# Optimization experiments

Measured on AMD Instinct MI355X. Metric: run time of the kernel, lower is better.

Reference implementation:

```python
import jax, jax.numpy as jnp
import numpy as np
from jax import lax

DILS = [2 ** i for i in range(11)] * 3  # 33 layers


def _conv1(x, w, b):
    # kernel_size=1 conv: w (O,I), x (B,I,T)
    return jnp.einsum('oi,bit->bot', w, x) + b[None, :, None]


def _dconv2(x, w, b, d):
    # kernel_size=2 dilated conv, torch padding='same': pad (d//2, d-d//2)
    y = lax.conv_general_dilated(
        x, w, window_strides=(1,), padding=[(d // 2, d - d // 2)],
        rhs_dilation=(d,), dimension_numbers=('NCH', 'OIH', 'NCH'))
    return y + b[None, :, None]


def setup_inputs() -> dict:
    key = jax.random.key(0)
    ks = jax.random.split(key, 7)
    B, T = 32, 16384
    s1 = 1.0           # fan_in=1*1
    s16 = 1.0 / np.sqrt(16.0)
    s16k2 = 1.0 / np.sqrt(16.0 * 2)
    s32 = 1.0 / np.sqrt(32.0)
    return {
        'x': jax.random.normal(ks[0], (B, 1, T), jnp.float32),
        'w1_first': jax.random.normal(ks[1], (16, 1), jnp.float32) * s1,
        'b1_first': jnp.zeros((16,), jnp.float32),
        'w1_post': jax.random.normal(ks[2], (32, 16, 16), jnp.float32) * s16,
        'b1_post': jnp.zeros((32, 16), jnp.float32),
        'wf': jax.random.normal(ks[3], (33, 32, 16, 2), jnp.float32) * s16k2,
        'bf': jnp.zeros((33, 32), jnp.float32),
        'wg': jax.random.normal(ks[4], (33, 32, 16, 2), jnp.float32) * s16k2,
        'bg': jnp.zeros((33, 32), jnp.float32),
        'w2': jax.random.normal(ks[5], (33, 16, 32), jnp.float32) * s32,
        'b2': jnp.zeros((33, 16), jnp.float32),
    }


def reference(x, w1_first, b1_first, w1_post, b1_post, wf, bf, wg, bg, w2, b2):
    skip_sum = 0.0
    for i, d in enumerate(DILS):
        if i == 0:
            x = jax.nn.relu(_conv1(x, w1_first, b1_first))
        else:
            x = jax.nn.relu(_conv1(x, w1_post[i - 1], b1_post[i - 1]))
        x_f = _dconv2(x, wf[i], bf[i], d)
        x_g = _dconv2(x, wg[i], bg[i], d)
        z = jnp.tanh(x_f) * jax.nn.sigmoid(x_g)
        z = jax.nn.relu(_conv1(z, w2[i], b2[i]))
        x = x + z
        skip_sum = skip_sum + z
    return jax.nn.relu(skip_sum)
```

## Files before the change

kernel.cpp:

```cpp
#include <hip/hip_runtime.h>

#define BB 32
#define TT 16384

typedef __attribute__((ext_vector_type(8))) short bf16x8;
typedef __attribute__((ext_vector_type(4))) float f32x4;
typedef __attribute__((ext_vector_type(4))) int i32x4;

#define MFMA(A, B, C) __builtin_amdgcn_mfma_f32_16x16x32_bf16((A), (B), (C), 0, 0, 0)

__device__ __forceinline__ unsigned short bf16_rne(float f) {
    unsigned int u = __float_as_uint(f);
    return (unsigned short)((u + 0x7FFF + ((u >> 16) & 1)) >> 16);
}
__device__ __forceinline__ float bf16_to_f(unsigned short h) {
    return __uint_as_float(((unsigned int)h) << 16);
}
__device__ __forceinline__ uint2 pk4(f32x4 v) {
    uint2 r;
    asm("v_cvt_pk_bf16_f32 %0, %1, %2" : "=v"(r.x) : "v"(v[0]), "v"(v[1]));
    asm("v_cvt_pk_bf16_f32 %0, %1, %2" : "=v"(r.y) : "v"(v[2]), "v"(v[3]));
    return r;
}

__device__ __forceinline__ float fast_sigmoid(float x) {
    float e = __expf(-x);
    return __builtin_amdgcn_rcpf(1.0f + e);
}
__device__ __forceinline__ float fast_tanh(float x) {
    float ax = fabsf(x);
    float e = __expf(2.0f * ax);
    float r = 1.0f - 2.0f * __builtin_amdgcn_rcpf(1.0f + e);
    return copysignf(r, x);
}

__global__ void prep_kernel(const float* __restrict__ w1_first,
                            const float* __restrict__ b1_first,
                            const float* __restrict__ w1_post,
                            const float* __restrict__ b1_post,
                            const float* __restrict__ wf, const float* __restrict__ bfb,
                            const float* __restrict__ wg, const float* __restrict__ bgb,
                            const float* __restrict__ w2, const float* __restrict__ b2,
                            short* __restrict__ Wfrag, float* __restrict__ Bset) {
    int L = blockIdx.x;
    int l = threadIdx.x;
    int op = l & 15;
    int q = l >> 4;
    int i0 = (q & 1) << 3;
    int tap = q >> 1;

    float gbuf[6][8];
#pragma unroll
    for (int j = 0; j < 8; ++j) {
        gbuf[0][j] = (L == 0) ? 0.f
                   : w1_post[((size_t)(L - 1) * 16 + op) * 16 + i0 + j];
        gbuf[1][j] = wf[(((size_t)L * 32 + op) * 16 + i0 + j) * 2 + tap];
        gbuf[2][j] = wf[(((size_t)L * 32 + 16 + op) * 16 + i0 + j) * 2 + tap];
        gbuf[3][j] = wg[(((size_t)L * 32 + op) * 16 + i0 + j) * 2 + tap];
        gbuf[4][j] = wg[(((size_t)L * 32 + 16 + op) * 16 + i0 + j) * 2 + tap];
        gbuf[5][j] = w2[((size_t)L * 16 + op) * 32 + (q << 3) + j];
    }

    constexpr int gsel[7] = {0, 0, 1, 2, 3, 4, 5};
    constexpr int hsel[7] = {1, 0, 1, 1, 1, 1, 1};
#pragma unroll
    for (int f = 0; f < 7; ++f) {
        size_t base = (((size_t)L * 7 + f) * 64 + l) * 8;
#pragma unroll
        for (int j = 0; j < 8; ++j) {
            float v = gbuf[gsel[f]][j];
            unsigned short h = bf16_rne(v);
            Wfrag[base + j] = hsel[f] ? (short)h
                                      : (short)bf16_rne(v - bf16_to_f(h));
        }
    }

#pragma unroll
    for (int r = 0; r < 4; ++r) {
        int c = (q << 2) + r;
        float bv[6];
        bv[0] = (L == 0) ? b1_first[c] : b1_post[(size_t)(L - 1) * 16 + c];
        bv[1] = bfb[(size_t)L * 32 + c];
        bv[2] = bfb[(size_t)L * 32 + 16 + c];
        bv[3] = bgb[(size_t)L * 32 + c];
        bv[4] = bgb[(size_t)L * 32 + 16 + c];
        bv[5] = b2[(size_t)L * 16 + c];
#pragma unroll
        for (int s = 0; s < 6; ++s)
            Bset[(((size_t)L * 6 + s) * 64 + l) * 4 + r] = bv[s];
    }
}

__device__ __forceinline__ f32x4 conv1_eval(bool first, const void* __restrict__ xin,
                                            const float* __restrict__ w1f,
                                            int b, int tp, int q,
                                            f32x4 b1v, bf16x8 A12) {
    const f32x4 zero = {0.f, 0.f, 0.f, 0.f};
    bool valid = ((unsigned)tp) < (unsigned)TT;
    f32x4 acc = valid ? b1v : zero;
    if (first) {
        const float* xf = (const float*)xin;
        float xv = valid ? xf[(size_t)b * TT + tp] : 0.f;
        const float4* w4 = (const float4*)w1f;
        float4 w = w4[q];
        acc[0] = fmaf(w.x, xv, acc[0]);
        acc[1] = fmaf(w.y, xv, acc[1]);
        acc[2] = fmaf(w.z, xv, acc[2]);
        acc[3] = fmaf(w.w, xv, acc[3]);
    } else {
        int tpc = valid ? tp : 0;
        const bf16x8 z8 = {0, 0, 0, 0, 0, 0, 0, 0};
        const bf16x8* xp = (const bf16x8*)((const char*)xin +
                            ((size_t)b * TT + tpc) * 32 + ((q & 1) << 4));
        bf16x8 bb = valid ? *xp : z8;
        acc = MFMA(A12, bb, acc);
    }
#pragma unroll
    for (int r = 0; r < 4; ++r) acc[r] = fmaxf(acc[r], 0.f);
    return acc;
}

template <int MODE>
__global__ __launch_bounds__(256) void wn_layer(
    const void* __restrict__ xin, void* __restrict__ xout,
    float* __restrict__ skip, float* __restrict__ dout,
    const short* __restrict__ WfragL, const float* __restrict__ BsetL,
    const float* __restrict__ w1f, int d) {
    __shared__ char sm[8192];

    const int tid = threadIdx.x;
    const int wave = tid >> 6, lane = tid & 63;
    const int p = lane & 15, q = lane >> 4;

    const int blk = ((blockIdx.x & 7) << 10) + (blockIdx.x >> 3);
    const int b = blk >> 8;
    const int tbase = ((blk & 255) << 6) + (wave << 4);
    const int pl = d >> 1, pr = d - pl;

    char* xrb = sm + wave * 1024;
    char* zb = sm + 4096 + wave * 1024;
    const int xorb = (p & 8) << 2;

    const bf16x8* WF = (const bf16x8*)WfragL;
    const f32x4* BS = (const f32x4*)BsetL;

    const f32x4 b1v = BS[lane];
    bf16x8 A12 = {0, 0, 0, 0, 0, 0, 0, 0};
    if (MODE != 1) A12 = (q < 2) ? WF[lane] : WF[64 + lane];

#pragma unroll
    for (int g = 0; g < 2; ++g) {
        int ts = tbase + (g ? pr : -pl);
        f32x4 xr = conv1_eval(MODE == 1, xin, w1f, b, ts + p, q, b1v, A12);
        *(uint2*)(xrb + (g << 9) +
                  ((((q >> 1) << 8) + (p << 4) + ((q & 1) << 3)) ^ xorb)) = pk4(xr);
    }

    f32x4 xrC = {0.f, 0.f, 0.f, 0.f};
    if (MODE != 2)
        xrC = conv1_eval(MODE == 1, xin, w1f, b, tbase + p, q, b1v, A12);

    bf16x8 bxr = *(const bf16x8*)(xrb + ((q >> 1) << 9) +
                                  ((((q & 1) << 8) + (p << 4)) ^ xorb));
    f32x4 f0 = MFMA(WF[2 * 64 + lane], bxr, BS[64 + lane]);
    f32x4 f1 = MFMA(WF[3 * 64 + lane], bxr, BS[128 + lane]);
    f32x4 g0 = MFMA(WF[4 * 64 + lane], bxr, BS[192 + lane]);
    f32x4 g1 = MFMA(WF[5 * 64 + lane], bxr, BS[256 + lane]);

    f32x4 z0, z1;
#pragma unroll
    for (int r = 0; r < 4; ++r) {
        z0[r] = fast_tanh(f0[r]) * fast_sigmoid(g0[r]);
        z1[r] = fast_tanh(f1[r]) * fast_sigmoid(g1[r]);
    }
    {
        int base = (((q >> 1) << 8) + (p << 4) + ((q & 1) << 3)) ^ xorb;
        *(uint2*)(zb + base) = pk4(z0);
        *(uint2*)(zb + 512 + base) = pk4(z1);
    }

    bf16x8 bz = *(const bf16x8*)(zb + (((q << 8) + (p << 4)) ^ xorb));
    f32x4 z2 = MFMA(WF[6 * 64 + lane], bz, BS[320 + lane]);
#pragma unroll
    for (int r = 0; r < 4; ++r) z2[r] = fmaxf(z2[r], 0.f);

    size_t pos = (size_t)b * TT + tbase + p;
    size_t xidx = (pos << 4) + (q << 2);
    if (MODE != 2) {
        f32x4 xo;
#pragma unroll
        for (int r = 0; r < 4; ++r) xo[r] = xrC[r] + z2[r];
        *(uint2*)((char*)xout + pos * 32 + (q << 3)) = pk4(xo);
        if (MODE == 1) {
            *(f32x4*)(skip + xidx) = z2;
        } else {
            f32x4 s = *(const f32x4*)(skip + xidx);
#pragma unroll
            for (int r = 0; r < 4; ++r) s[r] += z2[r];
            *(f32x4*)(skip + xidx) = s;
        }
    } else {
        f32x4 s = *(const f32x4*)(skip + xidx);
        size_t ob = (size_t)b * (16 * (size_t)TT) + (size_t)(q << 2) * TT + (tbase + p);
#pragma unroll
        for (int r = 0; r < 4; ++r)
            dout[ob + (size_t)r * TT] = fmaxf(s[r] + z2[r], 0.f);
    }
}

__global__ __launch_bounds__(256, 2) void wn_fused(
    const char* __restrict__ Xin, char* __restrict__ Xout,
    float* __restrict__ skip,
    const short* __restrict__ Wfrag, const float* __restrict__ Bset,
    int Lbase, int d0p, int NL) {
    extern __shared__ char sm[];
    char* Abuf = sm;
    char* Ubuf = sm + 24576;

    const int tid = threadIdx.x;
    const int wave = tid >> 6, lane = tid & 63;
    const int p = lane & 15, q = lane >> 4;
    char* zb = sm + 49152 + wave * 1024;
    const int xorb = (p & 8) << 2;

    const int gblk = ((blockIdx.x & 7) << 7) | (blockIdx.x >> 3);
    const int b = gblk >> 5;
    const int gt0 = ((gblk & 31) << 9) - 128;

#pragma unroll
    for (int jj = 0; jj < 3; ++jj) {
        int pos = jj * 256 + tid;
        int g = gt0 + pos;
        bool valid = ((unsigned)g) < (unsigned)TT;
        const char* src = Xin + ((size_t)b * TT + (valid ? g : 0)) * 32;
#pragma unroll
        for (int sub = 0; sub < 2; ++sub) {
            i32x4 v = {0, 0, 0, 0};
            if (valid) v = *(const i32x4*)(src + sub * 16);
            *(i32x4*)(Abuf + sub * 12288 + pos * 16) = v;
        }
    }
    __syncthreads();

    int uLo = 0, uHi = 48;
    f32x4 sk[8];
#pragma unroll
    for (int m = 0; m < 8; ++m) sk[m] = f32x4{0.f, 0.f, 0.f, 0.f};

#pragma unroll 1
    for (int k = 0; k < NL; ++k) {
        const int L = Lbase + k;
        const int d = 1 << (d0p + k);
        const int pl = d >> 1, pr = d - pl;
        const int tl = (pl + 15) >> 4, tr = (pr + 15) >> 4;
        const bool lastk = (k == NL - 1);
        const int nLo = uLo + tl, nHi = uHi - tr;

        const bf16x8* WF = (const bf16x8*)(Wfrag + (size_t)L * 7 * 64 * 8);
        const f32x4* BS = (const f32x4*)(Bset + (size_t)L * 6 * 64 * 4);
        const bf16x8 A12 = (q < 2) ? WF[lane] : WF[64 + lane];
        const bf16x8 Wf0 = WF[128 + lane], Wf1 = WF[192 + lane];
        const bf16x8 Wg0 = WF[256 + lane], Wg1 = WF[320 + lane];
        const bf16x8 W2f = WF[384 + lane];
        const f32x4 b1v = BS[lane];
        const f32x4 bf0 = BS[64 + lane], bf1 = BS[128 + lane];
        const f32x4 bg0 = BS[192 + lane], bg1 = BS[256 + lane];
        const f32x4 b2v = BS[320 + lane];

        f32x4 ureg[12];

#pragma unroll
        for (int m = 0; m < 12; ++m) {
            int T = 4 * m + wave;
            if (T >= uLo && T < uHi) {
                int pos = T * 16 + p;
                bf16x8 bb = *(const bf16x8*)(Abuf + (q & 1) * 12288 + pos * 16);
                f32x4 acc = b1v;
                acc = MFMA(A12, bb, acc);
                bool val = ((unsigned)(gt0 + pos)) < (unsigned)TT;
#pragma unroll
                for (int r = 0; r < 4; ++r)
                    acc[r] = val ? fmaxf(acc[r], 0.f) : 0.f;
                ureg[m] = acc;
                *(uint2*)(Ubuf + (q >> 1) * 12288 + pos * 16 + ((q & 1) << 3)) =
                    pk4(acc);
            }
        }
        __syncthreads();

#pragma unroll
        for (int m = 0; m < 12; ++m) {
            int T = 4 * m + wave;
            bool doit = lastk ? (m >= 2 && m <= 9) : (T >= nLo && T < nHi);
            if (doit) {
                int pos = T * 16 + p;
                int tap = (q >> 1) ? pr : -pl;
                bf16x8 bxr = *(const bf16x8*)(Ubuf + (q & 1) * 12288 + (pos + tap) * 16);
                f32x4 f0 = MFMA(Wf0, bxr, bf0);
                f32x4 f1 = MFMA(Wf1, bxr, bf1);
                f32x4 g0 = MFMA(Wg0, bxr, bg0);
                f32x4 g1 = MFMA(Wg1, bxr, bg1);

                f32x4 z0, z1;
#pragma unroll
                for (int r = 0; r < 4; ++r) {
                    z0[r] = fast_tanh(f0[r]) * fast_sigmoid(g0[r]);
                    z1[r] = fast_tanh(f1[r]) * fast_sigmoid(g1[r]);
                }
                int zbase = (((q >> 1) << 8) + (p << 4) + ((q & 1) << 3)) ^ xorb;
                *(uint2*)(zb + zbase) = pk4(z0);
                *(uint2*)(zb + 512 + zbase) = pk4(z1);
                bf16x8 bz = *(const bf16x8*)(zb + (((q << 8) + (p << 4)) ^ xorb));
                f32x4 z2 = MFMA(W2f, bz, b2v);
#pragma unroll
                for (int r = 0; r < 4; ++r) z2[r] = fmaxf(z2[r], 0.f);

                int g = gt0 + pos;
                f32x4 xo = ureg[m] + z2;

                if (!lastk) {
                    *(uint2*)(Abuf + (q >> 1) * 12288 + pos * 16 + ((q & 1) << 3)) =
                        pk4(xo);
                } else {
                    char* gx = Xout + ((size_t)b * TT + g) * 32;
                    *(uint2*)(gx + (q << 3)) = pk4(xo);
                }
                if (m >= 2 && m <= 9) sk[m - 2] += z2;
            }
        }
        __syncthreads();
        uLo = nLo;
        uHi = nHi;
    }

#pragma unroll
    for (int m = 2; m <= 9; ++m) {
        int T = 4 * m + wave;
        int g = gt0 + T * 16 + p;
        float* sp = skip + (((size_t)b * TT + g) << 4) + (q << 2);
        f32x4 s = *(const f32x4*)sp;
#pragma unroll
        for (int r = 0; r < 4; ++r) s[r] += sk[m - 2][r];
        *(f32x4*)sp = s;
    }
}

extern "C" void kernel_launch(void* const* d_in, const int* in_sizes, int n_in,
                              void* d_out, int out_size, void* d_ws, size_t ws_size,
                              hipStream_t stream) {
    const float* x        = (const float*)d_in[0];
    const float* w1_first = (const float*)d_in[1];
    const float* b1_first = (const float*)d_in[2];
    const float* w1_post  = (const float*)d_in[3];
    const float* b1_post  = (const float*)d_in[4];
    const float* wf       = (const float*)d_in[5];
    const float* bf       = (const float*)d_in[6];
    const float* wg       = (const float*)d_in[7];
    const float* bg       = (const float*)d_in[8];
    const float* w2       = (const float*)d_in[9];
    const float* b2       = (const float*)d_in[10];

    void* X0 = d_ws;
    float* SK = (float*)((char*)d_ws + 33554432);
    short* Wfrag = (short*)((char*)d_ws + 67108864);
    float* Bset = (float*)((char*)d_ws + 67345408);
    void* XD = d_out;
    float* dout = (float*)d_out;

    static bool attr_done = false;
    if (!attr_done) {
        hipFuncSetAttribute(reinterpret_cast<const void*>(wn_fused),
                            hipFuncAttributeMaxDynamicSharedMemorySize, 53248);
        attr_done = true;
    }

    prep_kernel<<<33, 64, 0, stream>>>(w1_first, b1_first, w1_post, b1_post,
                                       wf, bf, wg, bg, w2, b2, Wfrag, Bset);

    dim3 sblock(256), sgrid(BB * TT / 64);
    dim3 fblock(256);
    dim3 fgrid(BB * TT / 512);

    int n = 0;
    const void* cur_in = (const void*)x;
    auto nxt = [&](int parity) -> void* { return (parity & 1) ? XD : X0; };

    {
        void* out = nxt(n);
        wn_layer<1><<<sgrid, sblock, 0, stream>>>(cur_in, out, SK, dout,
                                                  Wfrag, Bset, w1_first, 1);
        cur_in = out; n ^= 1;
    }
    for (int cyc = 0; cyc < 3; ++cyc) {
        int Lb = (cyc == 0) ? 1 : 11 * cyc;
        int d0p = (cyc == 0) ? 1 : 0;
        int NL = (cyc == 0) ? 6 : 7;
        {
            void* out = nxt(n);
            wn_fused<<<fgrid, fblock, 53248, stream>>>(
                (const char*)cur_in, (char*)out, SK, Wfrag, Bset, Lb, d0p, NL);
            cur_in = out; n ^= 1;
        }
        int Ls = Lb + NL;
        for (int L = Ls; L <= Ls + 3; ++L) {
            int d = 1 << (L % 11);
            const short* WfL = Wfrag + (size_t)L * 7 * 64 * 8;
            const float* BsL = Bset + (size_t)L * 6 * 64 * 4;
            if (L == 32) {
                wn_layer<2><<<sgrid, sblock, 0, stream>>>(cur_in, nullptr, SK, dout,
                                                          WfL, BsL, w1_first, d);
            } else {
                void* out = nxt(n);
                wn_layer<0><<<sgrid, sblock, 0, stream>>>(cur_in, out, SK, dout,
                                                          WfL, BsL, w1_first, d);
                cur_in = out; n ^= 1;
            }
        }
    }
}
```

Before: 676.8 us.

## Double-buffer the 1x1-conv LDS tile to drop one barrier per layer

```diff
diff --git a/kernel.cpp b/kernel.cpp
--- a/kernel.cpp
+++ b/kernel.cpp
@@ -215,12 +215,11 @@
     int Lbase, int d0p, int NL) {
     extern __shared__ char sm[];
     char* Abuf = sm;
-    char* Ubuf = sm + 24576;
 
     const int tid = threadIdx.x;
     const int wave = tid >> 6, lane = tid & 63;
     const int p = lane & 15, q = lane >> 4;
-    char* zb = sm + 49152 + wave * 1024;
+    char* zb = sm + 73728 + wave * 1024;
     const int xorb = (p & 8) << 2;
 
     const int gblk = ((blockIdx.x & 7) << 7) | (blockIdx.x >> 3);
@@ -246,6 +245,33 @@
     f32x4 sk[8];
 #pragma unroll
     for (int m = 0; m < 8; ++m) sk[m] = f32x4{0.f, 0.f, 0.f, 0.f};
+
+    f32x4 ureg[12];
+
+    {
+        const bf16x8* WFn = (const bf16x8*)(Wfrag + (size_t)Lbase * 7 * 64 * 8);
+        const f32x4* BSn = (const f32x4*)(Bset + (size_t)Lbase * 6 * 64 * 4);
+        const bf16x8 A12 = (q < 2) ? WFn[lane] : WFn[64 + lane];
+        const f32x4 b1v = BSn[lane];
+        char* Uw = sm + 24576;
+#pragma unroll
+        for (int m = 0; m < 12; ++m) {
+            int T = 4 * m + wave;
+            if (T >= uLo && T < uHi) {
+                int pos = T * 16 + p;
+                bf16x8 bb = *(const bf16x8*)(Abuf + (q & 1) * 12288 + pos * 16);
+                f32x4 acc = b1v;
+                acc = MFMA(A12, bb, acc);
+                bool val = ((unsigned)(gt0 + pos)) < (unsigned)TT;
+#pragma unroll
+                for (int r = 0; r < 4; ++r)
+                    acc[r] = val ? fmaxf(acc[r], 0.f) : 0.f;
+                ureg[m] = acc;
+                *(uint2*)(Uw + (q >> 1) * 12288 + pos * 16 + ((q & 1) << 3)) =
+                    pk4(acc);
+            }
+        }
+    }
 
 #pragma unroll 1
     for (int k = 0; k < NL; ++k) {
@@ -258,34 +284,16 @@
 
         const bf16x8* WF = (const bf16x8*)(Wfrag + (size_t)L * 7 * 64 * 8);
         const f32x4* BS = (const f32x4*)(Bset + (size_t)L * 6 * 64 * 4);
-        const bf16x8 A12 = (q < 2) ? WF[lane] : WF[64 + lane];
         const bf16x8 Wf0 = WF[128 + lane], Wf1 = WF[192 + lane];
         const bf16x8 Wg0 = WF[256 + lane], Wg1 = WF[320 + lane];
         const bf16x8 W2f = WF[384 + lane];
-        const f32x4 b1v = BS[lane];
         const f32x4 bf0 = BS[64 + lane], bf1 = BS[128 + lane];
         const f32x4 bg0 = BS[192 + lane], bg1 = BS[256 + lane];
         const f32x4 b2v = BS[320 + lane];
 
-        f32x4 ureg[12];
-
-#pragma unroll
-        for (int m = 0; m < 12; ++m) {
-            int T = 4 * m + wave;
-            if (T >= uLo && T < uHi) {
-                int pos = T * 16 + p;
-                bf16x8 bb = *(const bf16x8*)(Abuf + (q & 1) * 12288 + pos * 16);
-                f32x4 acc = b1v;
-                acc = MFMA(A12, bb, acc);
-                bool val = ((unsigned)(gt0 + pos)) < (unsigned)TT;
-#pragma unroll
-                for (int r = 0; r < 4; ++r)
-                    acc[r] = val ? fmaxf(acc[r], 0.f) : 0.f;
-                ureg[m] = acc;
-                *(uint2*)(Ubuf + (q >> 1) * 12288 + pos * 16 + ((q & 1) << 3)) =
-                    pk4(acc);
-            }
-        }
+        char* Ur = sm + 24576 + (k & 1) * 24576;
+        char* Uw = sm + 24576 + ((k + 1) & 1) * 24576;
+
         __syncthreads();
 
 #pragma unroll
@@ -295,7 +303,7 @@
             if (doit) {
                 int pos = T * 16 + p;
                 int tap = (q >> 1) ? pr : -pl;
-                bf16x8 bxr = *(const bf16x8*)(Ubuf + (q & 1) * 12288 + (pos + tap) * 16);
+                bf16x8 bxr = *(const bf16x8*)(Ur + (q & 1) * 12288 + (pos + tap) * 16);
                 f32x4 f0 = MFMA(Wf0, bxr, bf0);
                 f32x4 f1 = MFMA(Wf1, bxr, bf1);
                 f32x4 g0 = MFMA(Wg0, bxr, bg0);
@@ -328,7 +336,30 @@
                 if (m >= 2 && m <= 9) sk[m - 2] += z2;
             }
         }
-        __syncthreads();
+
+        if (!lastk) {
+            const bf16x8* WFn = (const bf16x8*)(Wfrag + (size_t)(L + 1) * 7 * 64 * 8);
+            const f32x4* BSn = (const f32x4*)(Bset + (size_t)(L + 1) * 6 * 64 * 4);
+            const bf16x8 A12n = (q < 2) ? WFn[lane] : WFn[64 + lane];
+            const f32x4 b1vn = BSn[lane];
+#pragma unroll
+            for (int m = 0; m < 12; ++m) {
+                int T = 4 * m + wave;
+                if (T >= nLo && T < nHi) {
+                    int pos = T * 16 + p;
+                    bf16x8 bb = *(const bf16x8*)(Abuf + (q & 1) * 12288 + pos * 16);
+                    f32x4 acc = b1vn;
+                    acc = MFMA(A12n, bb, acc);
+                    bool val = ((unsigned)(gt0 + pos)) < (unsigned)TT;
+#pragma unroll
+                    for (int r = 0; r < 4; ++r)
+                        acc[r] = val ? fmaxf(acc[r], 0.f) : 0.f;
+                    ureg[m] = acc;
+                    *(uint2*)(Uw + (q >> 1) * 12288 + pos * 16 + ((q & 1) << 3)) =
+                        pk4(acc);
+                }
+            }
+        }
         uLo = nLo;
         uHi = nHi;
     }
@@ -370,7 +401,7 @@
     static bool attr_done = false;
     if (!attr_done) {
         hipFuncSetAttribute(reinterpret_cast<const void*>(wn_fused),
-                            hipFuncAttributeMaxDynamicSharedMemorySize, 53248);
+                            hipFuncAttributeMaxDynamicSharedMemorySize, 77824);
         attr_done = true;
     }
 
@@ -397,7 +428,7 @@
         int NL = (cyc == 0) ? 6 : 7;
         {
             void* out = nxt(n);
-            wn_fused<<<fgrid, fblock, 53248, stream>>>(
+            wn_fused<<<fgrid, fblock, 77824, stream>>>(
                 (const char*)cur_in, (char*)out, SK, Wfrag, Bset, Lb, d0p, NL);
             cur_in = out; n ^= 1;
         }
```

After: 668.0 us, median of 2. About the same (-1.3%).
